# Kernel optimization log

Hardware: AMD Instinct MI355X
Metric: run time of the kernel (lower is better)

The kernel has to match this reference:

```python
import jax, jax.numpy as jnp
import numpy as np
from itertools import product

N_VOX = 100000
GRID = 128
KS = 3
K = KS ** 3
INC_MAX, OUTC_MAX = 64, 96
RUNTIME_INC, RUNTIME_OUTC = 48, 64


def _build_rulebook(rng):
    flat = rng.choice(GRID ** 3, size=N_VOX, replace=False).astype(np.int64)
    coords = np.stack(np.unravel_index(flat, (GRID, GRID, GRID)), axis=1)  # [N,3]
    # Dense lookup table: flat coord -> voxel index (or -1).
    table = np.full(GRID ** 3, -1, dtype=np.int32)
    table[flat] = np.arange(N_VOX, dtype=np.int32)
    offsets = np.array(list(product([-1, 0, 1], repeat=3)), dtype=np.int64)  # [27,3]
    idx = np.empty((K, N_VOX), dtype=np.int32)
    for k, off in enumerate(offsets):
        nb = coords + off  # stride=1, dilation=1
        valid = np.all((nb >= 0) & (nb < GRID), axis=1)
        nb_flat = (nb[:, 0] * GRID + nb[:, 1]) * GRID + nb[:, 2]
        nb_flat = np.where(valid, nb_flat, 0)
        idx[k] = np.where(valid, table[nb_flat], -1)
    return idx


def setup_inputs() -> dict:
    key = jax.random.key(0)
    kf, kw = jax.random.split(key)
    features = jax.random.normal(kf, (N_VOX, RUNTIME_INC), dtype=jnp.float32)
    # Full kernel param [K, inc_max, outc_max]; runtime-sliced inside reference.
    std = 1.0 / np.sqrt(INC_MAX * K)
    kernel = jax.random.uniform(kw, (K, INC_MAX, OUTC_MAX), dtype=jnp.float32,
                                minval=-std, maxval=std)
    idx = jnp.asarray(_build_rulebook(np.random.default_rng(0)))  # [K, N]
    return {"features": features, "kernel": kernel, "idx": idx,
            "runtime_inc": RUNTIME_INC, "runtime_outc": RUNTIME_OUTC}


def reference(features, kernel, idx, runtime_inc, runtime_outc):
    # Dynamic channel slicing (static Python ints -> jit friendly).
    w = kernel[:, :runtime_inc, :runtime_outc]          # [K, Ci, Co]
    mask = idx >= 0                                      # [K, N]
    safe = jnp.where(mask, idx, 0)
    # Gather -> per-offset GEMM -> accumulate (scatter is identity: out idx == n).
    gathered = features[safe] * mask[..., None].astype(features.dtype)  # [K, N, Ci]
    out = jnp.einsum('knc,kco->no', gathered, w)         # [N, Co]
    return out
```

## Files before the change

### kernel.cpp

```cpp
#include <hip/hip_runtime.h>
#include <hip/hip_bf16.h>


#define NVOX       100000
#define INC        48
#define INC_MAX    64
#define OUTC       64
#define OUTC_MAX   96
#define KOFF       27
#define FEAT_ROW   64
#define FEATB_ELEMS ((NVOX + 1) * FEAT_ROW)
#define WTB_K      3072
#define WTB_ELEMS  (KOFF * WTB_K)
#define WS_NEED    ((size_t)(FEATB_ELEMS + WTB_ELEMS) * 2)
#define FEAT_THREADS ((NVOX + 1) * 8)
#define FEAT_PREP_BLKS ((FEAT_THREADS + 255) / 256)
#define WTB_PREP_BLKS  (WTB_ELEMS / 256)
#define MAIN_BLOCKS 782

typedef __attribute__((ext_vector_type(8)))  short short8;
typedef __attribute__((ext_vector_type(4)))  float floatx4;
typedef __attribute__((ext_vector_type(16))) float floatx16;

__device__ __forceinline__ short f2bf(float f) {
    union { __hip_bfloat16 h; short s; } u;
    u.h = __float2bfloat16(f);
    return u.s;
}

__global__ void __launch_bounds__(256)
prep_cvt(const float* __restrict__ feat, const float* __restrict__ wk,
         short* __restrict__ featb, short* __restrict__ wtb)
{
    int b = blockIdx.x;
    if (b < FEAT_PREP_BLKS) {
        int t = b * 256 + threadIdx.x;
        if (t < FEAT_THREADS) {
            int g = t >> 3, c8 = (t & 7) * 8;
            short8 p = (short8){0, 0, 0, 0, 0, 0, 0, 0};
            if (g < NVOX && c8 < INC) {
                const floatx4* src = (const floatx4*)(feat + g * INC + c8);
                floatx4 f0 = src[0], f1 = src[1];
                #pragma unroll
                for (int j = 0; j < 4; ++j) { p[j] = f2bf(f0[j]); p[4 + j] = f2bf(f1[j]); }
            }
            *(short8*)(featb + g * FEAT_ROW + c8) = p;
        }
    } else {
        int t = (b - FEAT_PREP_BLKS) * 256 + threadIdx.x;
        int k = t / WTB_K, r = t % WTB_K;
        int chunk = r >> 3, j = r & 7;
        int f = chunk >> 6, lane = chunk & 63;
        int ks = f >> 1, nt = f & 1;
        int c = ks * 16 + (lane >> 5) * 8 + j;
        int o = nt * 32 + (lane & 31);
        wtb[t] = f2bf(wk[k * (INC_MAX * OUTC_MAX) + c * OUTC_MAX + o]);
    }
}

__global__ void __launch_bounds__(256, 3)
spconv_main(const short* __restrict__ featb, const short* __restrict__ wtb,
            const int* __restrict__ idx, float* __restrict__ out)
{
    __shared__ short Bs[4][WTB_K];

    const int tid  = threadIdx.x;
    const int lane = tid & 63;
    const int wave = tid >> 6;
    const int l32  = lane & 31;
    const int hi   = lane >> 5;

    int bid = blockIdx.x;
    int sb  = (bid < 776) ? ((bid & 7) * 97 + (bid >> 3)) : bid;

    const int m0   = (sb * 4 + wave) * 32;
    const bool act = (m0 < NVOX);
    const int rr   = act ? (m0 + l32) : 0;

    floatx16 acc[2];
    #pragma unroll
    for (int nt = 0; nt < 2; ++nt)
        #pragma unroll
        for (int r = 0; r < 16; ++r) acc[nt][r] = 0.f;

    short8 A[2][3];
    short8 bst[2][2];
    int    rowg[4];

    auto ldrow = [&](int k) {
        int t0 = idx[k * NVOX + rr];
        rowg[k & 3] = (t0 < 0) ? NVOX : t0;
    };
    auto aload = [&](int k) {
        const short* p = featb + rowg[k & 3] * FEAT_ROW + hi * 8;
        A[k & 1][0] = *(const short8*)(p);
        A[k & 1][1] = *(const short8*)(p + 16);
        A[k & 1][2] = *(const short8*)(p + 32);
    };
    auto bload = [&](int k) {
        bst[k & 1][0] = *(const short8*)(wtb + k * WTB_K + tid * 8);
        if (tid < 128)
            bst[k & 1][1] = *(const short8*)(wtb + k * WTB_K + 2048 + tid * 8);
    };
    auto compute = [&](int k) {
        #pragma unroll
        for (int ks = 0; ks < 3; ++ks) {
            short8 b0 = *(const short8*)&Bs[k & 3][(ks * 128 + lane) * 8];
            short8 b1 = *(const short8*)&Bs[k & 3][(ks * 128 + 64 + lane) * 8];
            acc[0] = __builtin_amdgcn_mfma_f32_32x32x16_bf16(
                A[k & 1][ks], b0, acc[0], 0, 0, 0);
            acc[1] = __builtin_amdgcn_mfma_f32_32x32x16_bf16(
                A[k & 1][ks], b1, acc[1], 0, 0, 0);
        }
    };

    ldrow(0); ldrow(1); ldrow(2); ldrow(3);
    bload(0); bload(1);
    aload(0); aload(1);

    #pragma unroll
    for (int j = 0; j < 14; ++j) {
        const int kk = 2 * j;

        *(short8*)&Bs[kk & 3][tid * 8] = bst[0][0];
        if (tid < 128) *(short8*)&Bs[kk & 3][2048 + tid * 8] = bst[0][1];
        if (kk + 1 < KOFF) {
            *(short8*)&Bs[(kk + 1) & 3][tid * 8] = bst[1][0];
            if (tid < 128) *(short8*)&Bs[(kk + 1) & 3][2048 + tid * 8] = bst[1][1];
        }
        __syncthreads();

        if (kk + 2 < KOFF) bload(kk + 2);
        if (kk + 3 < KOFF) bload(kk + 3);
        if (kk + 4 < KOFF) ldrow(kk + 4);
        if (kk + 5 < KOFF) ldrow(kk + 5);

        compute(kk);
        if (kk + 2 < KOFF) aload(kk + 2);
        if (kk + 1 < KOFF) {
            compute(kk + 1);
            if (kk + 3 < KOFF) aload(kk + 3);
        }
    }

    if (act) {
        #pragma unroll
        for (int nt = 0; nt < 2; ++nt) {
            #pragma unroll
            for (int r = 0; r < 16; ++r) {
                int row = (r & 3) + 8 * (r >> 2) + 4 * hi;
                out[(m0 + row) * OUTC + nt * 32 + l32] = acc[nt][r];
            }
        }
    }
}

__global__ void __launch_bounds__(256)
spconv_fallback(const float* __restrict__ feat, const float* __restrict__ wk,
                const int* __restrict__ idx, float* __restrict__ out)
{
    int t = blockIdx.x * 256 + threadIdx.x;
    if (t >= NVOX * OUTC) return;
    int n = t >> 6, o = t & 63;
    float s = 0.f;
    for (int k = 0; k < KOFF; ++k) {
        int g = idx[k * NVOX + n];
        if (g >= 0) {
            const float* fr = feat + g * INC;
            const float* wr = wk + k * (INC_MAX * OUTC_MAX) + o;
            #pragma unroll 8
            for (int c = 0; c < INC; ++c) s += fr[c] * wr[c * OUTC_MAX];
        }
    }
    out[t] = s;
}

extern "C" void kernel_launch(void* const* d_in, const int* in_sizes, int n_in,
                              void* d_out, int out_size, void* d_ws, size_t ws_size,
                              hipStream_t stream) {
    const float* feat = (const float*)d_in[0];
    const float* wk   = (const float*)d_in[1];
    const int*   idx  = (const int*)d_in[2];
    float* out = (float*)d_out;

    if (ws_size >= WS_NEED) {
        short* featb = (short*)d_ws;
        short* wtb   = featb + FEATB_ELEMS;
        prep_cvt<<<FEAT_PREP_BLKS + WTB_PREP_BLKS, 256, 0, stream>>>(feat, wk, featb, wtb);
        spconv_main<<<MAIN_BLOCKS, 256, 0, stream>>>(featb, wtb, idx, out);
    } else {
        spconv_fallback<<<(NVOX * OUTC + 255) / 256, 256, 0, stream>>>(feat, wk, idx, out);
    }
}
```

Before: 109.3 us.

## Gather fp32 features directly and convert in-register, drop bf16 feature prep pass

Removes the separate pass that converted all features to a padded bf16 buffer. The main kernel now gathers fp32 rows directly, with a zero row for missing neighbours, and converts them to bf16 in registers. Weights are read straight from global/L2 instead of being staged through LDS with __syncthreads. Each wave now handles 64 rows in two 32-row groups that reuse the same weight fragments, and offsets where no lane has a neighbour are skipped. The cost is twice the gather bytes per feature row, a simpler loop with less software prefetch, and higher register pressure.

```diff
diff --git a/kernel.cpp b/kernel.cpp
--- a/kernel.cpp
+++ b/kernel.cpp
@@ -1,6 +1,5 @@
 #include <hip/hip_runtime.h>
 #include <hip/hip_bf16.h>
-
 
 #define NVOX       100000
 #define INC        48
@@ -8,13 +7,10 @@
 #define OUTC       64
 #define OUTC_MAX   96
 #define KOFF       27
-#define FEAT_ROW   64
-#define FEATB_ELEMS ((NVOX + 1) * FEAT_ROW)
 #define WTB_K      3072
 #define WTB_ELEMS  (KOFF * WTB_K)
-#define WS_NEED    ((size_t)(FEATB_ELEMS + WTB_ELEMS) * 2)
-#define FEAT_THREADS ((NVOX + 1) * 8)
-#define FEAT_PREP_BLKS ((FEAT_THREADS + 255) / 256)
+#define ZROW_FLOATS 48
+#define WS_NEED    ((size_t)WTB_ELEMS * 2 + ZROW_FLOATS * 4)
 #define WTB_PREP_BLKS  (WTB_ELEMS / 256)
 #define MAIN_BLOCKS 782
 
@@ -29,25 +25,12 @@
 }
 
 __global__ void __launch_bounds__(256)
-prep_cvt(const float* __restrict__ feat, const float* __restrict__ wk,
-         short* __restrict__ featb, short* __restrict__ wtb)
+prep_w(const float* __restrict__ wk, short* __restrict__ wtb,
+       float* __restrict__ zrowf)
 {
     int b = blockIdx.x;
-    if (b < FEAT_PREP_BLKS) {
+    if (b < WTB_PREP_BLKS) {
         int t = b * 256 + threadIdx.x;
-        if (t < FEAT_THREADS) {
-            int g = t >> 3, c8 = (t & 7) * 8;
-            short8 p = (short8){0, 0, 0, 0, 0, 0, 0, 0};
-            if (g < NVOX && c8 < INC) {
-                const floatx4* src = (const floatx4*)(feat + g * INC + c8);
-                floatx4 f0 = src[0], f1 = src[1];
-                #pragma unroll
-                for (int j = 0; j < 4; ++j) { p[j] = f2bf(f0[j]); p[4 + j] = f2bf(f1[j]); }
-            }
-            *(short8*)(featb + g * FEAT_ROW + c8) = p;
-        }
-    } else {
-        int t = (b - FEAT_PREP_BLKS) * 256 + threadIdx.x;
         int k = t / WTB_K, r = t % WTB_K;
         int chunk = r >> 3, j = r & 7;
         int f = chunk >> 6, lane = chunk & 63;
@@ -55,15 +38,16 @@
         int c = ks * 16 + (lane >> 5) * 8 + j;
         int o = nt * 32 + (lane & 31);
         wtb[t] = f2bf(wk[k * (INC_MAX * OUTC_MAX) + c * OUTC_MAX + o]);
+    } else if (threadIdx.x < ZROW_FLOATS) {
+        zrowf[threadIdx.x] = 0.f;
     }
 }
 
-__global__ void __launch_bounds__(256, 3)
-spconv_main(const short* __restrict__ featb, const short* __restrict__ wtb,
-            const int* __restrict__ idx, float* __restrict__ out)
+__global__ void __launch_bounds__(128, 2)
+spconv_main(const float* __restrict__ feat, const short* __restrict__ wtb,
+            const float* __restrict__ zrowf, const int* __restrict__ idx,
+            float* __restrict__ out)
 {
-    __shared__ short Bs[4][WTB_K];
-
     const int tid  = threadIdx.x;
     const int lane = tid & 63;
     const int wave = tid >> 6;
@@ -73,85 +57,84 @@
     int bid = blockIdx.x;
     int sb  = (bid < 776) ? ((bid & 7) * 97 + (bid >> 3)) : bid;
 
-    const int m0   = (sb * 4 + wave) * 32;
-    const bool act = (m0 < NVOX);
-    const int rr   = act ? (m0 + l32) : 0;
+    const int m0 = (sb * 2 + wave) * 64;
+    if (m0 >= NVOX) return;
+    const bool act1 = (m0 + 32) < NVOX;
+    const int r0 = m0 + l32;
+    const int r1 = act1 ? (m0 + 32 + l32) : 0;
 
-    floatx16 acc[2];
+    floatx16 acc[2][2];
+    #pragma unroll
+    for (int g = 0; g < 2; ++g)
+        #pragma unroll
+        for (int nt = 0; nt < 2; ++nt)
+            #pragma unroll
+            for (int r = 0; r < 16; ++r) acc[g][nt][r] = 0.f;
+
+    int t0 = idx[r0];
+    int t1 = act1 ? idx[r1] : -1;
+
+    #pragma unroll 1
+    for (int k = 0; k < KOFF; ++k) {
+        int n0 = -1, n1 = -1;
+        if (k + 1 < KOFF) {
+            n0 = idx[(k + 1) * NVOX + r0];
+            if (act1) n1 = idx[(k + 1) * NVOX + r1];
+        }
+        const bool v0 = (t0 >= 0), v1 = (t1 >= 0);
+        if (__any(v0 || v1)) {
+            const float* a0p = v0 ? (feat + t0 * INC) : zrowf;
+            const float* a1p = v1 ? (feat + t1 * INC) : zrowf;
+
+            const short8* bp = (const short8*)(wtb + k * WTB_K);
+            short8 bw[3][2];
+            #pragma unroll
+            for (int ks = 0; ks < 3; ++ks) {
+                bw[ks][0] = bp[ks * 128 + lane];
+                bw[ks][1] = bp[ks * 128 + 64 + lane];
+            }
+            floatx4 f0[3][2], f1[3][2];
+            #pragma unroll
+            for (int ks = 0; ks < 3; ++ks) {
+                const floatx4* p0 = (const floatx4*)(a0p + ks * 16 + hi * 8);
+                const floatx4* p1 = (const floatx4*)(a1p + ks * 16 + hi * 8);
+                f0[ks][0] = p0[0]; f0[ks][1] = p0[1];
+                f1[ks][0] = p1[0]; f1[ks][1] = p1[1];
+            }
+            #pragma unroll
+            for (int ks = 0; ks < 3; ++ks) {
+                short8 a0, a1;
+                #pragma unroll
+                for (int j = 0; j < 4; ++j) {
+                    a0[j]     = f2bf(f0[ks][0][j]);
+                    a0[4 + j] = f2bf(f0[ks][1][j]);
+                    a1[j]     = f2bf(f1[ks][0][j]);
+                    a1[4 + j] = f2bf(f1[ks][1][j]);
+                }
+                acc[0][0] = __builtin_amdgcn_mfma_f32_32x32x16_bf16(a0, bw[ks][0], acc[0][0], 0, 0, 0);
+                acc[0][1] = __builtin_amdgcn_mfma_f32_32x32x16_bf16(a0, bw[ks][1], acc[0][1], 0, 0, 0);
+                acc[1][0] = __builtin_amdgcn_mfma_f32_32x32x16_bf16(a1, bw[ks][0], acc[1][0], 0, 0, 0);
+                acc[1][1] = __builtin_amdgcn_mfma_f32_32x32x16_bf16(a1, bw[ks][1], acc[1][1], 0, 0, 0);
+            }
+        }
+        t0 = n0; t1 = n1;
+    }
+
     #pragma unroll
     for (int nt = 0; nt < 2; ++nt)
         #pragma unroll
-        for (int r = 0; r < 16; ++r) acc[nt][r] = 0.f;
-
-    short8 A[2][3];
-    short8 bst[2][2];
-    int    rowg[4];
-
-    auto ldrow = [&](int k) {
-        int t0 = idx[k * NVOX + rr];
-        rowg[k & 3] = (t0 < 0) ? NVOX : t0;
-    };
-    auto aload = [&](int k) {
-        const short* p = featb + rowg[k & 3] * FEAT_ROW + hi * 8;
-        A[k & 1][0] = *(const short8*)(p);
-        A[k & 1][1] = *(const short8*)(p + 16);
-        A[k & 1][2] = *(const short8*)(p + 32);
-    };
-    auto bload = [&](int k) {
-        bst[k & 1][0] = *(const short8*)(wtb + k * WTB_K + tid * 8);
-        if (tid < 128)
-            bst[k & 1][1] = *(const short8*)(wtb + k * WTB_K + 2048 + tid * 8);
-    };
-    auto compute = [&](int k) {
+        for (int r = 0; r < 16; ++r) {
+            int row = (r & 3) + 8 * (r >> 2) + 4 * hi;
+            out[(m0 + row) * OUTC + nt * 32 + l32] = acc[0][nt][r];
+        }
+    if (act1) {
         #pragma unroll
-        for (int ks = 0; ks < 3; ++ks) {
-            short8 b0 = *(const short8*)&Bs[k & 3][(ks * 128 + lane) * 8];
-            short8 b1 = *(const short8*)&Bs[k & 3][(ks * 128 + 64 + lane) * 8];
-            acc[0] = __builtin_amdgcn_mfma_f32_32x32x16_bf16(
-                A[k & 1][ks], b0, acc[0], 0, 0, 0);
-            acc[1] = __builtin_amdgcn_mfma_f32_32x32x16_bf16(
-                A[k & 1][ks], b1, acc[1], 0, 0, 0);
-        }
-    };
-
-    ldrow(0); ldrow(1); ldrow(2); ldrow(3);
-    bload(0); bload(1);
-    aload(0); aload(1);
-
-    #pragma unroll
-    for (int j = 0; j < 14; ++j) {
-        const int kk = 2 * j;
-
-        *(short8*)&Bs[kk & 3][tid * 8] = bst[0][0];
-        if (tid < 128) *(short8*)&Bs[kk & 3][2048 + tid * 8] = bst[0][1];
-        if (kk + 1 < KOFF) {
-            *(short8*)&Bs[(kk + 1) & 3][tid * 8] = bst[1][0];
-            if (tid < 128) *(short8*)&Bs[(kk + 1) & 3][2048 + tid * 8] = bst[1][1];
-        }
-        __syncthreads();
-
-        if (kk + 2 < KOFF) bload(kk + 2);
-        if (kk + 3 < KOFF) bload(kk + 3);
-        if (kk + 4 < KOFF) ldrow(kk + 4);
-        if (kk + 5 < KOFF) ldrow(kk + 5);
-
-        compute(kk);
-        if (kk + 2 < KOFF) aload(kk + 2);
-        if (kk + 1 < KOFF) {
-            compute(kk + 1);
-            if (kk + 3 < KOFF) aload(kk + 3);
-        }
-    }
-
-    if (act) {
-        #pragma unroll
-        for (int nt = 0; nt < 2; ++nt) {
+        for (int nt = 0; nt < 2; ++nt)
             #pragma unroll
             for (int r = 0; r < 16; ++r) {
                 int row = (r & 3) + 8 * (r >> 2) + 4 * hi;
-                out[(m0 + row) * OUTC + nt * 32 + l32] = acc[nt][r];
+                out[(m0 + 32 + row) * OUTC + nt * 32 + l32] = acc[1][nt][r];
             }
-        }
     }
 }
 
@@ -184,10 +167,10 @@
     float* out = (float*)d_out;
 
     if (ws_size >= WS_NEED) {
-        short* featb = (short*)d_ws;
-        short* wtb   = featb + FEATB_ELEMS;
-        prep_cvt<<<FEAT_PREP_BLKS + WTB_PREP_BLKS, 256, 0, stream>>>(feat, wk, featb, wtb);
-        spconv_main<<<MAIN_BLOCKS, 256, 0, stream>>>(featb, wtb, idx, out);
+        short* wtb   = (short*)d_ws;
+        float* zrowf = (float*)((char*)d_ws + (size_t)WTB_ELEMS * 2);
+        prep_w<<<WTB_PREP_BLKS + 1, 256, 0, stream>>>(wk, wtb, zrowf);
+        spconv_main<<<MAIN_BLOCKS, 128, 0, stream>>>(feat, wtb, zrowf, idx, out);
     } else {
         spconv_fallback<<<(NVOX * OUTC + 255) / 256, 256, 0, stream>>>(feat, wk, idx, out);
     }
```

Result: slower. 132.7 us (+21.3%).

## Gather fp32 features directly in main kernel and skip empty-offset MFMAs

Applied to the files above, without the earlier changes.

Removes the feature pre-conversion pass to a padded bf16 buffer. The main kernel now gathers fp32 rows straight from the input and converts them to bf16 in registers before each MFMA, with a small zero row standing in for missing neighbors. It also skips the loads and MFMAs for an offset when no lane in the wave has a valid neighbor. The trade-off is twice the gather bytes per row and more register pressure from holding fp32 fragments, and the wave-uniform skip only helps when a whole 32-row tile lacks a given neighbor.

```diff
diff --git a/kernel.cpp b/kernel.cpp
--- a/kernel.cpp
+++ b/kernel.cpp
@@ -1,6 +1,5 @@
 #include <hip/hip_runtime.h>
 #include <hip/hip_bf16.h>
-
 
 #define NVOX       100000
 #define INC        48
@@ -8,13 +7,10 @@
 #define OUTC       64
 #define OUTC_MAX   96
 #define KOFF       27
-#define FEAT_ROW   64
-#define FEATB_ELEMS ((NVOX + 1) * FEAT_ROW)
 #define WTB_K      3072
 #define WTB_ELEMS  (KOFF * WTB_K)
-#define WS_NEED    ((size_t)(FEATB_ELEMS + WTB_ELEMS) * 2)
-#define FEAT_THREADS ((NVOX + 1) * 8)
-#define FEAT_PREP_BLKS ((FEAT_THREADS + 255) / 256)
+#define ZROW_FLOATS 48
+#define WS_NEED    ((size_t)WTB_ELEMS * 2 + ZROW_FLOATS * 4)
 #define WTB_PREP_BLKS  (WTB_ELEMS / 256)
 #define MAIN_BLOCKS 782
 
@@ -29,25 +25,12 @@
 }
 
 __global__ void __launch_bounds__(256)
-prep_cvt(const float* __restrict__ feat, const float* __restrict__ wk,
-         short* __restrict__ featb, short* __restrict__ wtb)
+prep_w(const float* __restrict__ wk, short* __restrict__ wtb,
+       float* __restrict__ zrowf)
 {
     int b = blockIdx.x;
-    if (b < FEAT_PREP_BLKS) {
+    if (b < WTB_PREP_BLKS) {
         int t = b * 256 + threadIdx.x;
-        if (t < FEAT_THREADS) {
-            int g = t >> 3, c8 = (t & 7) * 8;
-            short8 p = (short8){0, 0, 0, 0, 0, 0, 0, 0};
-            if (g < NVOX && c8 < INC) {
-                const floatx4* src = (const floatx4*)(feat + g * INC + c8);
-                floatx4 f0 = src[0], f1 = src[1];
-                #pragma unroll
-                for (int j = 0; j < 4; ++j) { p[j] = f2bf(f0[j]); p[4 + j] = f2bf(f1[j]); }
-            }
-            *(short8*)(featb + g * FEAT_ROW + c8) = p;
-        }
-    } else {
-        int t = (b - FEAT_PREP_BLKS) * 256 + threadIdx.x;
         int k = t / WTB_K, r = t % WTB_K;
         int chunk = r >> 3, j = r & 7;
         int f = chunk >> 6, lane = chunk & 63;
@@ -55,12 +38,15 @@
         int c = ks * 16 + (lane >> 5) * 8 + j;
         int o = nt * 32 + (lane & 31);
         wtb[t] = f2bf(wk[k * (INC_MAX * OUTC_MAX) + c * OUTC_MAX + o]);
+    } else if (threadIdx.x < ZROW_FLOATS) {
+        zrowf[threadIdx.x] = 0.f;
     }
 }
 
 __global__ void __launch_bounds__(256, 3)
-spconv_main(const short* __restrict__ featb, const short* __restrict__ wtb,
-            const int* __restrict__ idx, float* __restrict__ out)
+spconv_main(const float* __restrict__ feat, const short* __restrict__ wtb,
+            const float* __restrict__ zrowf, const int* __restrict__ idx,
+            float* __restrict__ out)
 {
     __shared__ short Bs[4][WTB_K];
 
@@ -83,19 +69,30 @@
         #pragma unroll
         for (int r = 0; r < 16; ++r) acc[nt][r] = 0.f;
 
-    short8 A[2][3];
-    short8 bst[2][2];
-    int    rowg[4];
+    floatx4 F[2][3][2];
+    short8  bst[2][2];
+    int     rowg[4];
+    bool    va4[4];
+    bool    ca[2];
 
     auto ldrow = [&](int k) {
         int t0 = idx[k * NVOX + rr];
-        rowg[k & 3] = (t0 < 0) ? NVOX : t0;
+        rowg[k & 3] = t0;
+        va4[k & 3] = __any(t0 >= 0);
     };
     auto aload = [&](int k) {
-        const short* p = featb + rowg[k & 3] * FEAT_ROW + hi * 8;
-        A[k & 1][0] = *(const short8*)(p);
-        A[k & 1][1] = *(const short8*)(p + 16);
-        A[k & 1][2] = *(const short8*)(p + 32);
+        bool v = va4[k & 3];
+        ca[k & 1] = v;
+        if (v) {
+            int t = rowg[k & 3];
+            const float* p = (t >= 0) ? (feat + (size_t)t * INC) : zrowf;
+            #pragma unroll
+            for (int ks = 0; ks < 3; ++ks) {
+                const floatx4* q = (const floatx4*)(p + ks * 16 + hi * 8);
+                F[k & 1][ks][0] = q[0];
+                F[k & 1][ks][1] = q[1];
+            }
+        }
     };
     auto bload = [&](int k) {
         bst[k & 1][0] = *(const short8*)(wtb + k * WTB_K + tid * 8);
@@ -103,14 +100,19 @@
             bst[k & 1][1] = *(const short8*)(wtb + k * WTB_K + 2048 + tid * 8);
     };
     auto compute = [&](int k) {
+        if (!ca[k & 1]) return;
         #pragma unroll
         for (int ks = 0; ks < 3; ++ks) {
             short8 b0 = *(const short8*)&Bs[k & 3][(ks * 128 + lane) * 8];
             short8 b1 = *(const short8*)&Bs[k & 3][(ks * 128 + 64 + lane) * 8];
-            acc[0] = __builtin_amdgcn_mfma_f32_32x32x16_bf16(
-                A[k & 1][ks], b0, acc[0], 0, 0, 0);
-            acc[1] = __builtin_amdgcn_mfma_f32_32x32x16_bf16(
-                A[k & 1][ks], b1, acc[1], 0, 0, 0);
+            short8 a;
+            #pragma unroll
+            for (int j = 0; j < 4; ++j) {
+                a[j]     = f2bf(F[k & 1][ks][0][j]);
+                a[4 + j] = f2bf(F[k & 1][ks][1][j]);
+            }
+            acc[0] = __builtin_amdgcn_mfma_f32_32x32x16_bf16(a, b0, acc[0], 0, 0, 0);
+            acc[1] = __builtin_amdgcn_mfma_f32_32x32x16_bf16(a, b1, acc[1], 0, 0, 0);
         }
     };
 
@@ -184,10 +186,10 @@
     float* out = (float*)d_out;
 
     if (ws_size >= WS_NEED) {
-        short* featb = (short*)d_ws;
-        short* wtb   = featb + FEATB_ELEMS;
-        prep_cvt<<<FEAT_PREP_BLKS + WTB_PREP_BLKS, 256, 0, stream>>>(feat, wk, featb, wtb);
-        spconv_main<<<MAIN_BLOCKS, 256, 0, stream>>>(featb, wtb, idx, out);
+        short* wtb   = (short*)d_ws;
+        float* zrowf = (float*)((char*)d_ws + (size_t)WTB_ELEMS * 2);
+        prep_w<<<WTB_PREP_BLKS + 1, 256, 0, stream>>>(wk, wtb, zrowf);
+        spconv_main<<<MAIN_BLOCKS, 256, 0, stream>>>(feat, wtb, zrowf, idx, out);
     } else {
         spconv_fallback<<<(NVOX * OUTC + 255) / 256, 256, 0, stream>>>(feat, wk, idx, out);
     }
```

New measurement: 110.4 us. About the same (+1.0%).
